# Kernel optimization log

Measured on AMD Instinct MI355X. Metric: run time of the kernel, lower is better.

## Reference

```python
import math
import jax, jax.numpy as jnp
import numpy as np

N_HEADS = 16
HIDDEN = 1024
FACTOR = 256
N_DK = HIDDEN // N_HEADS
B, S = 4, 2048


def _linear_params(key, fan_in, fan_out):
    kw, kb = jax.random.split(key)
    bound = 1.0 / math.sqrt(fan_in)
    W = jax.random.uniform(kw, (fan_in, fan_out), jnp.float32, -bound, bound)
    b = jax.random.uniform(kb, (fan_out,), jnp.float32, -bound, bound)
    return W, b


def setup_inputs() -> dict:
    key = jax.random.key(0)
    ks = jax.random.split(key, 12)
    inp = {
        "query": jax.random.normal(ks[0], (B, S, HIDDEN), jnp.float32),
        "key": jax.random.normal(ks[1], (B, S, HIDDEN), jnp.float32),
        "value": jax.random.normal(ks[2], (B, S, HIDDEN), jnp.float32),
        "mask": jax.random.randint(ks[3], (B, S), 0, 2, jnp.int32),
    }
    names = [("pq", HIDDEN, FACTOR), ("tq", FACTOR, HIDDEN),
             ("pk", HIDDEN, FACTOR), ("tk", FACTOR, HIDDEN),
             ("pv", HIDDEN, FACTOR), ("tv", FACTOR, HIDDEN),
             ("po", HIDDEN, FACTOR), ("to", FACTOR, HIDDEN)]
    for i, (nm, fi, fo) in enumerate(names):
        W, b = _linear_params(ks[4 + i], fi, fo)
        inp[f"W{nm}"], inp[f"b{nm}"] = W, b
    return inp


def _factored(x, Wp, bp, Wt, bt):
    # proj -> leaky_relu(0.2) -> tran
    h = jax.nn.leaky_relu(x @ Wp + bp, negative_slope=0.2)
    return h @ Wt + bt


def reference(query, key, value, mask,
              Wpq, bpq, Wtq, btq, Wpk, bpk, Wtk, btk,
              Wpv, bpv, Wtv, btv, Wpo, bpo, Wto, bto):
    bsize = query.shape[0]

    def split_heads(x):  # [B,S,H*Dk] -> [B,H,S,Dk]
        return x.reshape(bsize, -1, N_HEADS, N_DK).transpose(0, 2, 1, 3)

    q = split_heads(_factored(query, Wpq, bpq, Wtq, btq))
    k = split_heads(_factored(key, Wpk, bpk, Wtk, btk))
    v = split_heads(_factored(value, Wpv, bpv, Wtv, btv))

    scores = jnp.einsum("bhqd,bhkd->bhqk", q, k) / math.sqrt(N_DK)
    m = (mask == 0)[:, None, None, :]  # [B,1,1,S]
    scores = jnp.where(m, jnp.float32(-1e20), scores)
    attn = jax.nn.softmax(scores, axis=-1)
    cv = jnp.einsum("bhqk,bhkd->bhqd", attn, v)
    cv = cv.transpose(0, 2, 1, 3).reshape(bsize, -1, N_HEADS * N_DK)
    # dropout omitted (eval mode / deterministic reference)
    return _factored(cv, Wpo, bpo, Wto, bto)
```

## Files before the change

kernel.cpp:

```cpp
#include <hip/hip_runtime.h>
#include <cstdint>
#include <cstddef>

typedef __bf16 bf16_t;
typedef __bf16 bf16x8 __attribute__((ext_vector_type(8)));
typedef float  f32x4  __attribute__((ext_vector_type(4)));
typedef unsigned int uint32x4 __attribute__((ext_vector_type(4)));

#define DEV_INLINE __device__ __forceinline__

constexpr int Bsz = 4, Ssz = 2048, HID = 1024, FAC = 256, NH = 16, DKc = 64;
constexpr int Mrows = Bsz * Ssz;
constexpr float QSCALE = 0.18033688011112042f;

struct Ptr8 { const float* p[8]; };
struct Ptr3 { const float* p[3]; };

DEV_INLINE float fast_exp2(float x) {
#if __has_builtin(__builtin_amdgcn_exp2f)
  return __builtin_amdgcn_exp2f(x);
#else
  return exp2f(x);
#endif
}

DEV_INLINE void async16(const void* g, void* l) {
  __builtin_amdgcn_global_load_lds((const __attribute__((address_space(1))) void*)g,
                                   (__attribute__((address_space(3))) void*)l, 16, 0, 0);
}

DEV_INLINE int SW(int r) { return (r & 3) | ((r >> 1) & 4); }

__global__ __launch_bounds__(256) void k_prep_w(Ptr8 s, bf16_t* wpt, bf16_t* wtt) {
  const int z = blockIdx.z;
  const int K = (z < 4) ? HID : FAC;
  const int N = (z < 4) ? FAC : HID;
  if ((int)(blockIdx.x * 32) >= N || (int)(blockIdx.y * 32) >= K) return;
  __shared__ float t[32][33];
  const float* src = s.p[z];
  bf16_t* dst = (z < 4) ? (wpt + (size_t)z * FAC * HID) : (wtt + (size_t)(z - 4) * FAC * HID);
  const int tx = threadIdx.x & 31, ty = threadIdx.x >> 5;
  const int kb = blockIdx.y * 32, nb = blockIdx.x * 32;
#pragma unroll
  for (int j = 0; j < 4; ++j)
    t[ty + j * 8][tx] = src[(size_t)(kb + ty + j * 8) * N + nb + tx];
  __syncthreads();
#pragma unroll
  for (int j = 0; j < 4; ++j)
    dst[(size_t)(nb + ty + j * 8) * K + kb + tx] = (bf16_t)t[tx][ty + j * 8];
}

__global__ __launch_bounds__(256) void k_pack_bias(Ptr8 s, const int* __restrict__ mask,
                                                   float* bp, float* bt, float* mf, bf16_t* mb) {
  const int tid = threadIdx.x;
  for (int i = tid; i < 4 * FAC; i += 256) bp[i] = s.p[i >> 8][i & 255];
  for (int i = tid; i < 4 * HID; i += 256) bt[i] = s.p[4 + (i >> 10)][i & 1023];
  for (int i = tid; i < Bsz * Ssz; i += 256) {
    const float m = (mask[i] != 0) ? 1.f : 0.f;
    mf[i] = m;
    mb[i] = (bf16_t)m;
  }
}

__global__ __launch_bounds__(256) void k_tv(const bf16_t* __restrict__ src, bf16_t* __restrict__ dst) {
  constexpr int LDT = 72;
  __shared__ __align__(16) bf16_t T[64 * LDT];
  const int st = blockIdx.x, h = blockIdx.y, b = blockIdx.z;
  const int tid = threadIdx.x;
  const int sr = tid >> 3, sc8 = (tid & 7) * 8;
  const size_t g0 = (size_t)(b * Ssz + st * 64 + sr) * HID + h * DKc + sc8;
  *(uint32x4*)(T + sr * LDT + sc8) = *(const uint32x4*)(src + g0);
  *(uint32x4*)(T + (sr + 32) * LDT + sc8) = *(const uint32x4*)(src + g0 + (size_t)32 * HID);
  __syncthreads();
  union { bf16_t e[8]; uint32x4 u; } o0, o1;
#pragma unroll
  for (int j = 0; j < 8; ++j) {
    o0.e[j] = T[(sc8 + j) * LDT + sr];
    o1.e[j] = T[(sc8 + j) * LDT + sr + 32];
  }
  const size_t d0 = ((size_t)(b * NH + h) * DKc + sr) * Ssz + st * 64 + sc8;
  *(uint32x4*)(dst + d0) = o0.u;
  *(uint32x4*)(dst + d0 + (size_t)32 * Ssz) = o1.u;
}

template <int CAST_A, int ACT, int RM, typename OUT_T>
__global__ __launch_bounds__(256) void k_gemm(Ptr3 Asrc,
                                              const bf16_t* __restrict__ Aall,
                                              const bf16_t* __restrict__ Btall,
                                              const float* __restrict__ biasAll,
                                              OUT_T* __restrict__ Call,
                                              OUT_T* __restrict__ C2,
                                              const float* __restrict__ rowmul,
                                              int N, int K,
                                              long long Az, long long Bz, long long Cz, int biasz,
                                              float sc0, float sc1, float sc2) {
  constexpr int LDTA = CAST_A ? 40 : 32;
  __shared__ __align__(16) bf16_t As[128 * LDTA];
  __shared__ __align__(16) bf16_t Bs[128 * 32];

  const int z = blockIdx.z;
  const bf16_t* Bt = Btall + (size_t)z * Bz;
  const float* bias = biasAll + (size_t)z * biasz;
  OUT_T* C = (z == 2 && C2) ? C2 : (Call + (size_t)z * Cz);
  const float scale = (z == 0) ? sc0 : ((z == 1) ? sc1 : sc2);

  const int tid = threadIdx.x;
  const int lane = tid & 63, wave = tid >> 6;
  const int quad = lane >> 4, l16 = lane & 15;
  const int wr = wave >> 1, wc = wave & 1;
  const int m0 = blockIdx.y * 128, n0 = blockIdx.x * 128;

  const int arow = wave * 16 + (lane >> 2), akc = (lane & 3) * 8;
  const bf16_t* gB0 = Bt + (size_t)(n0 + arow) * K + akc;
  const bf16_t* gB1 = gB0 + (size_t)64 * K;
  bf16_t* lB0 = Bs + wave * 512;
  bf16_t* lB1 = Bs + 2048 + wave * 512;

  const bf16_t* gA0 = nullptr; const bf16_t* gA1 = nullptr;
  bf16_t* lA0 = As + wave * 512;
  bf16_t* lA1 = As + 2048 + wave * 512;
  const float* gAf = nullptr;
  bf16_t* lAc = nullptr;
  if (CAST_A) {
    const int crow = tid >> 1, chalf = (tid & 1) * 16;
    gAf = Asrc.p[z] + (size_t)(m0 + crow) * K + chalf;
    lAc = As + crow * LDTA + chalf;
  } else {
    const bf16_t* A = Aall + (size_t)z * Az;
    gA0 = A + (size_t)(m0 + arow) * K + akc;
    gA1 = gA0 + (size_t)64 * K;
  }

  f32x4 acc[4][4] = {};

  for (int k0 = 0; k0 < K; k0 += 32) {
    async16(gB0 + k0, lB0);
    async16(gB1 + k0, lB1);
    if (CAST_A) {
      f32x4 x0 = *(const f32x4*)(gAf + k0);
      f32x4 x1 = *(const f32x4*)(gAf + k0 + 4);
      f32x4 x2 = *(const f32x4*)(gAf + k0 + 8);
      f32x4 x3 = *(const f32x4*)(gAf + k0 + 12);
      union { bf16_t h[16]; uint32x4 u[2]; } o;
#pragma unroll
      for (int j = 0; j < 4; ++j) {
        o.h[j] = (bf16_t)x0[j]; o.h[4 + j] = (bf16_t)x1[j];
        o.h[8 + j] = (bf16_t)x2[j]; o.h[12 + j] = (bf16_t)x3[j];
      }
      *(uint32x4*)lAc = o.u[0];
      *(uint32x4*)(lAc + 8) = o.u[1];
    } else {
      async16(gA0 + k0, lA0);
      async16(gA1 + k0, lA1);
    }
    __syncthreads();

    bf16x8 af[4], bfr[4];
#pragma unroll
    for (int i = 0; i < 4; ++i)
      af[i] = *(const bf16x8*)(As + (wr * 64 + i * 16 + l16) * LDTA + quad * 8);
#pragma unroll
    for (int i = 0; i < 4; ++i)
      bfr[i] = *(const bf16x8*)(Bs + (wc * 64 + i * 16 + l16) * 32 + quad * 8);
#pragma unroll
    for (int mi = 0; mi < 4; ++mi)
#pragma unroll
      for (int ni = 0; ni < 4; ++ni)
        acc[mi][ni] = __builtin_amdgcn_mfma_f32_16x16x32_bf16(af[mi], bfr[ni], acc[mi][ni], 0, 0, 0);
    if (k0 + 32 < K) __syncthreads();
  }

#pragma unroll
  for (int mi = 0; mi < 4; ++mi) {
    const int rbase = m0 + wr * 64 + mi * 16 + quad * 4;
    float rmv[4] = {1.f, 1.f, 1.f, 1.f};
    if (RM && z == 2) {
#pragma unroll
      for (int r = 0; r < 4; ++r) rmv[r] = rowmul[rbase + r];
    }
#pragma unroll
    for (int ni = 0; ni < 4; ++ni) {
      const int col = n0 + wc * 64 + ni * 16 + l16;
      const float bv = bias[col];
#pragma unroll
      for (int r = 0; r < 4; ++r) {
        float y = acc[mi][ni][r] + bv;
        if (ACT == 1) y = (y > 0.f) ? y : 0.2f * y;
        y *= scale * rmv[r];
        C[(size_t)(rbase + r) * N + col] = (OUT_T)y;
      }
    }
  }
}

__global__ __launch_bounds__(256, 4) void k_attn(const bf16_t* __restrict__ qkv,
                                                 const bf16_t* __restrict__ mb,
                                                 bf16_t* __restrict__ cv) {
  __shared__ __align__(16) bf16_t Ks[2][64 * 64];
  __shared__ __align__(16) bf16_t Vt[2][64 * 64];
  __shared__ __align__(16) bf16_t Ml[Ssz];

  const int qt = blockIdx.x, h = blockIdx.y, b = blockIdx.z;
  const bf16_t* qp = qkv;
  const bf16_t* kp = qkv + (size_t)Mrows * HID;
  const bf16_t* vtp = qkv + 2 * (size_t)Mrows * HID + (size_t)(b * NH + h) * DKc * Ssz;

  const int tid = threadIdx.x;
  const int lane = tid & 63, wave = tid >> 6;
  const int quad = lane >> 4, l16 = lane & 15;

  const int r0 = wave * 16 + (lane >> 3);
  const int r1 = r0 + 8;
  const int c0 = ((lane & 7) ^ SW(r0)) * 8;
  const int c1 = ((lane & 7) ^ SW(r1)) * 8;
  const int ldsOff = wave * 1024;
  const bf16_t* kgA = kp + (size_t)(b * Ssz + r0) * HID + h * DKc + c0;
  const bf16_t* kgB = kp + (size_t)(b * Ssz + r1) * HID + h * DKc + c1;
  const bf16_t* vgA = vtp + (size_t)r0 * Ssz + c0;
  const bf16_t* vgB = vtp + (size_t)r1 * Ssz + c1;

  *(uint32x4*)(Ml + tid * 8) = *(const uint32x4*)(mb + (size_t)b * Ssz + tid * 8);
  async16(kgA, Ks[0] + ldsOff);
  async16(kgB, Ks[0] + ldsOff + 512);
  async16(vgA, Vt[0] + ldsOff);
  async16(vgB, Vt[0] + ldsOff + 512);

  bf16x8 aq0[2], aq1[2];
#pragma unroll
  for (int g = 0; g < 2; ++g) {
    const size_t qrow = (size_t)(b * Ssz + qt * 128 + g * 64 + wave * 16 + l16) * HID + h * DKc + quad * 8;
    aq0[g] = *(const bf16x8*)(qp + qrow);
    aq1[g] = *(const bf16x8*)(qp + qrow + 32);
  }
  __syncthreads();

  const int krow = 8 * (l16 >> 2) + (l16 & 3);
  f32x4 acc[2][4] = {};
  f32x4 dacc[2] = {};
  const bf16x8 zfrag = {};

  for (int kt = 0; kt < 32; ++kt) {
    const int cur = kt & 1, nxt = cur ^ 1;
    if (kt < 31) {
      const size_t ko = (size_t)(kt + 1) * 64 * HID;
      const int vo = (kt + 1) * 64;
      async16(kgA + ko, Ks[nxt] + ldsOff);
      async16(kgB + ko, Ks[nxt] + ldsOff + 512);
      async16(vgA + vo, Vt[nxt] + ldsOff);
      async16(vgB + vo, Vt[nxt] + ldsOff + 512);
    }

    uint32_t pk[2][8];
    constexpr int koff[4] = {0, 4, 32, 36};
#pragma unroll
    for (int ks = 0; ks < 4; ++ks) {
      const int row = krow + koff[ks];
      const int sw = SW(row);
      bf16x8 a0 = *(const bf16x8*)(Ks[cur] + row * 64 + (quad ^ sw) * 8);
      bf16x8 a1 = *(const bf16x8*)(Ks[cur] + row * 64 + ((quad + 4) ^ sw) * 8);
#pragma unroll
      for (int g = 0; g < 2; ++g) {
        f32x4 c = {};
        c = __builtin_amdgcn_mfma_f32_16x16x32_bf16(a0, aq0[g], c, 0, 0, 0);
        c = __builtin_amdgcn_mfma_f32_16x16x32_bf16(a1, aq1[g], c, 0, 0, 0);
        union { bf16_t h[2]; uint32_t u; } p01, p23;
        p01.h[0] = (bf16_t)fast_exp2(c[0]);
        p01.h[1] = (bf16_t)fast_exp2(c[1]);
        p23.h[0] = (bf16_t)fast_exp2(c[2]);
        p23.h[1] = (bf16_t)fast_exp2(c[3]);
        pk[g][ks * 2] = p01.u;
        pk[g][ks * 2 + 1] = p23.u;
      }
    }
    union { uint32x4 u; bf16x8 h; } ap0[2], ap1[2];
#pragma unroll
    for (int g = 0; g < 2; ++g) {
      ap0[g].u = uint32x4{pk[g][0], pk[g][1], pk[g][2], pk[g][3]};
      ap1[g].u = uint32x4{pk[g][4], pk[g][5], pk[g][6], pk[g][7]};
    }

    bf16x8 mr0 = *(const bf16x8*)(Ml + kt * 64 + quad * 8);
    bf16x8 mr1 = *(const bf16x8*)(Ml + kt * 64 + 32 + quad * 8);
    if (l16 != 0) { mr0 = zfrag; mr1 = zfrag; }
#pragma unroll
    for (int g = 0; g < 2; ++g) {
      dacc[g] = __builtin_amdgcn_mfma_f32_16x16x32_bf16(ap0[g].h, mr0, dacc[g], 0, 0, 0);
      dacc[g] = __builtin_amdgcn_mfma_f32_16x16x32_bf16(ap1[g].h, mr1, dacc[g], 0, 0, 0);
    }

#pragma unroll
    for (int d = 0; d < 4; ++d) {
      const int row = d * 16 + l16;
      const int sw = SW(row);
      bf16x8 bv0 = *(const bf16x8*)(Vt[cur] + row * 64 + (quad ^ sw) * 8);
      bf16x8 bv1 = *(const bf16x8*)(Vt[cur] + row * 64 + ((quad + 4) ^ sw) * 8);
#pragma unroll
      for (int g = 0; g < 2; ++g) {
        acc[g][d] = __builtin_amdgcn_mfma_f32_16x16x32_bf16(ap0[g].h, bv0, acc[g][d], 0, 0, 0);
        acc[g][d] = __builtin_amdgcn_mfma_f32_16x16x32_bf16(ap1[g].h, bv1, acc[g][d], 0, 0, 0);
      }
    }

    __syncthreads();
  }

#pragma unroll
  for (int g = 0; g < 2; ++g) {
    const size_t obase = (size_t)(b * Ssz + qt * 128 + g * 64 + wave * 16 + quad * 4) * HID + h * DKc + l16;
#pragma unroll
    for (int r = 0; r < 4; ++r) {
      const float denom = __shfl(dacc[g][r], lane & 48, 64);
      const float rl = 1.f / denom;
#pragma unroll
      for (int d = 0; d < 4; ++d)
        cv[obase + (size_t)r * HID + d * 16] = (bf16_t)(acc[g][d][r] * rl);
    }
  }
}

extern "C" void kernel_launch(void* const* d_in, const int* in_sizes, int n_in,
                              void* d_out, int out_size, void* d_ws, size_t ws_size,
                              hipStream_t stream) {
  (void)in_sizes; (void)n_in; (void)out_size; (void)ws_size;
  const float* q_in = (const float*)d_in[0];
  const float* k_in = (const float*)d_in[1];
  const float* v_in = (const float*)d_in[2];
  const int* mask = (const int*)d_in[3];

  bf16_t* XB = (bf16_t*)d_ws;
  bf16_t* H3 = XB + (size_t)3 * Mrows * HID;
  bf16_t* CV = H3 + (size_t)3 * Mrows * FAC;
  bf16_t* WPT = CV + (size_t)Mrows * HID;
  bf16_t* WTT = WPT + (size_t)4 * FAC * HID;
  float* BP = (float*)(WTT + (size_t)4 * FAC * HID);
  float* BT = BP + 4 * FAC;
  float* MF = BT + 4 * HID;
  bf16_t* MB = (bf16_t*)(MF + Mrows);
  bf16_t* VTg = XB + 2 * (size_t)Mrows * HID;

  Ptr8 w;
  w.p[0] = (const float*)d_in[4];  w.p[1] = (const float*)d_in[8];
  w.p[2] = (const float*)d_in[12]; w.p[3] = (const float*)d_in[16];
  w.p[4] = (const float*)d_in[6];  w.p[5] = (const float*)d_in[10];
  w.p[6] = (const float*)d_in[14]; w.p[7] = (const float*)d_in[18];
  hipLaunchKernelGGL(k_prep_w, dim3(32, 32, 8), dim3(256), 0, stream, w, WPT, WTT);

  Ptr8 bs;
  bs.p[0] = (const float*)d_in[5];  bs.p[1] = (const float*)d_in[9];
  bs.p[2] = (const float*)d_in[13]; bs.p[3] = (const float*)d_in[17];
  bs.p[4] = (const float*)d_in[7];  bs.p[5] = (const float*)d_in[11];
  bs.p[6] = (const float*)d_in[15]; bs.p[7] = (const float*)d_in[19];
  hipLaunchKernelGGL(k_pack_bias, dim3(1), dim3(256), 0, stream, bs, mask, BP, BT, MF, MB);

  Ptr3 xs; xs.p[0] = q_in; xs.p[1] = k_in; xs.p[2] = v_in;
  Ptr3 nullp; nullp.p[0] = nullp.p[1] = nullp.p[2] = nullptr;

  hipLaunchKernelGGL((k_gemm<1, 1, 0, bf16_t>), dim3(FAC / 128, Mrows / 128, 3), dim3(256), 0, stream,
                     xs, (const bf16_t*)nullptr, WPT, BP, H3, (bf16_t*)nullptr, (const float*)nullptr,
                     FAC, HID, 0LL, (long long)FAC * HID, (long long)Mrows * FAC, FAC,
                     1.f, 1.f, 1.f);

  hipLaunchKernelGGL((k_gemm<0, 0, 1, bf16_t>), dim3(HID / 128, Mrows / 128, 3), dim3(256), 0, stream,
                     nullp, H3, WTT, BT, XB, CV, MF,
                     HID, FAC, (long long)Mrows * FAC, (long long)FAC * HID, (long long)Mrows * HID, HID,
                     QSCALE, 1.f, 1.f);

  hipLaunchKernelGGL(k_tv, dim3(Ssz / 64, NH, Bsz), dim3(256), 0, stream, CV, VTg);

  hipLaunchKernelGGL(k_attn, dim3(Ssz / 128, NH, Bsz), dim3(256), 0, stream, XB, MB, CV);

  hipLaunchKernelGGL((k_gemm<0, 1, 0, bf16_t>), dim3(FAC / 128, Mrows / 128, 1), dim3(256), 0, stream,
                     nullp, CV, WPT + (size_t)3 * FAC * HID, BP + 3 * FAC, H3, (bf16_t*)nullptr,
                     (const float*)nullptr, FAC, HID, 0LL, 0LL, 0LL, 0, 1.f, 1.f, 1.f);

  hipLaunchKernelGGL((k_gemm<0, 0, 0, float>), dim3(HID / 128, Mrows / 128, 1), dim3(256), 0, stream,
                     nullp, H3, WTT + (size_t)3 * FAC * HID, BT + 3 * HID, (float*)d_out, (float*)nullptr,
                     (const float*)nullptr, HID, FAC, 0LL, 0LL, 0LL, 0, 1.f, 1.f, 1.f);
}
```

Before: 378.9 us.

## Add double-buffered 64-row GEMM for K=1024 projections and parallelize bias packing

```diff
diff --git a/kernel.cpp b/kernel.cpp
--- a/kernel.cpp
+++ b/kernel.cpp
@@ -52,10 +52,10 @@
 
 __global__ __launch_bounds__(256) void k_pack_bias(Ptr8 s, const int* __restrict__ mask,
                                                    float* bp, float* bt, float* mf, bf16_t* mb) {
-  const int tid = threadIdx.x;
-  for (int i = tid; i < 4 * FAC; i += 256) bp[i] = s.p[i >> 8][i & 255];
-  for (int i = tid; i < 4 * HID; i += 256) bt[i] = s.p[4 + (i >> 10)][i & 1023];
-  for (int i = tid; i < Bsz * Ssz; i += 256) {
+  const int i = blockIdx.x * 256 + threadIdx.x;
+  if (i < 4 * FAC) bp[i] = s.p[i >> 8][i & 255];
+  if (i < 4 * HID) bt[i] = s.p[4 + (i >> 10)][i & 1023];
+  if (i < Bsz * Ssz) {
     const float m = (mask[i] != 0) ? 1.f : 0.f;
     mf[i] = m;
     mb[i] = (bf16_t)m;
@@ -83,9 +83,111 @@
   *(uint32x4*)(dst + d0 + (size_t)32 * Ssz) = o1.u;
 }
 
-template <int CAST_A, int ACT, int RM, typename OUT_T>
-__global__ __launch_bounds__(256) void k_gemm(Ptr3 Asrc,
-                                              const bf16_t* __restrict__ Aall,
+template <int CAST_A, typename OUT_T>
+__global__ __launch_bounds__(256) void k_gemmP(Ptr3 Asrc,
+                                               const bf16_t* __restrict__ Aall,
+                                               const bf16_t* __restrict__ Bt_,
+                                               const float* __restrict__ biasAll,
+                                               OUT_T* __restrict__ Call,
+                                               int K,
+                                               long long Az, long long Bz, long long Cz, int biasz) {
+  constexpr int LDTA = CAST_A ? 40 : 32;
+  __shared__ __align__(16) bf16_t As[2][64 * LDTA];
+  __shared__ __align__(16) bf16_t Bs[2][128 * 32];
+
+  const int z = blockIdx.z;
+  const bf16_t* Bt = Bt_ + (size_t)z * Bz;
+  const float* bias = biasAll + (size_t)z * biasz;
+  OUT_T* C = Call + (size_t)z * Cz;
+
+  const int tid = threadIdx.x;
+  const int lane = tid & 63, wave = tid >> 6;
+  const int quad = lane >> 4, l16 = lane & 15;
+  const int m0 = blockIdx.y * 64, n0 = blockIdx.x * 128;
+
+  const int arow = wave * 16 + (lane >> 2), akc = (lane & 3) * 8;
+  const bf16_t* gB0 = Bt + (size_t)(n0 + arow) * K + akc;
+  const bf16_t* gB1 = gB0 + (size_t)64 * K;
+
+  const float* gAf = nullptr;
+  const bf16_t* gA = nullptr;
+  const int crow = tid >> 2, chalf = (tid & 3) * 8;
+  if (CAST_A) gAf = Asrc.p[z] + (size_t)(m0 + crow) * K + chalf;
+  else        gA  = Aall + (size_t)z * Az + (size_t)(m0 + arow) * K + akc;
+
+  async16(gB0, Bs[0] + wave * 512);
+  async16(gB1, Bs[0] + 2048 + wave * 512);
+  if (CAST_A) {
+    f32x4 x0 = *(const f32x4*)gAf;
+    f32x4 x1 = *(const f32x4*)(gAf + 4);
+    union { bf16_t h[8]; uint32x4 u; } o;
+#pragma unroll
+    for (int j = 0; j < 4; ++j) { o.h[j] = (bf16_t)x0[j]; o.h[4 + j] = (bf16_t)x1[j]; }
+    *(uint32x4*)(As[0] + crow * LDTA + chalf) = o.u;
+  } else {
+    async16(gA, As[0] + wave * 512);
+  }
+
+  f32x4 acc[4][2] = {};
+  const int nk = K / 32;
+
+  for (int it = 0; it < nk; ++it) {
+    const int cur = it & 1, nxt = cur ^ 1;
+    __syncthreads();
+
+    f32x4 xa, xb;
+    const int k1 = (it + 1) * 32;
+    if (it + 1 < nk) {
+      async16(gB0 + k1, Bs[nxt] + wave * 512);
+      async16(gB1 + k1, Bs[nxt] + 2048 + wave * 512);
+      if (CAST_A) {
+        xa = *(const f32x4*)(gAf + k1);
+        xb = *(const f32x4*)(gAf + k1 + 4);
+      } else {
+        async16(gA + k1, As[nxt] + wave * 512);
+      }
+    }
+
+    bf16x8 af[4], bfr[2];
+#pragma unroll
+    for (int i = 0; i < 4; ++i)
+      af[i] = *(const bf16x8*)(As[cur] + (i * 16 + l16) * LDTA + quad * 8);
+#pragma unroll
+    for (int i = 0; i < 2; ++i)
+      bfr[i] = *(const bf16x8*)(Bs[cur] + (wave * 32 + i * 16 + l16) * 32 + quad * 8);
+#pragma unroll
+    for (int mi = 0; mi < 4; ++mi)
+#pragma unroll
+      for (int ni = 0; ni < 2; ++ni)
+        acc[mi][ni] = __builtin_amdgcn_mfma_f32_16x16x32_bf16(af[mi], bfr[ni], acc[mi][ni], 0, 0, 0);
+
+    if (CAST_A && it + 1 < nk) {
+      union { bf16_t h[8]; uint32x4 u; } o;
+#pragma unroll
+      for (int j = 0; j < 4; ++j) { o.h[j] = (bf16_t)xa[j]; o.h[4 + j] = (bf16_t)xb[j]; }
+      *(uint32x4*)(As[nxt] + crow * LDTA + chalf) = o.u;
+    }
+  }
+
+#pragma unroll
+  for (int mi = 0; mi < 4; ++mi) {
+    const int rbase = m0 + mi * 16 + quad * 4;
+#pragma unroll
+    for (int ni = 0; ni < 2; ++ni) {
+      const int col = n0 + wave * 32 + ni * 16 + l16;
+      const float bv = bias[col];
+#pragma unroll
+      for (int r = 0; r < 4; ++r) {
+        float y = acc[mi][ni][r] + bv;
+        y = (y > 0.f) ? y : 0.2f * y;
+        C[(size_t)(rbase + r) * FAC + col] = (OUT_T)y;
+      }
+    }
+  }
+}
+
+template <int ACT, int RM, typename OUT_T>
+__global__ __launch_bounds__(256) void k_gemm(const bf16_t* __restrict__ Aall,
                                               const bf16_t* __restrict__ Btall,
                                               const float* __restrict__ biasAll,
                                               OUT_T* __restrict__ Call,
@@ -94,8 +196,7 @@
                                               int N, int K,
                                               long long Az, long long Bz, long long Cz, int biasz,
                                               float sc0, float sc1, float sc2) {
-  constexpr int LDTA = CAST_A ? 40 : 32;
-  __shared__ __align__(16) bf16_t As[128 * LDTA];
+  __shared__ __align__(16) bf16_t As[128 * 32];
   __shared__ __align__(16) bf16_t Bs[128 * 32];
 
   const int z = blockIdx.z;
@@ -116,49 +217,25 @@
   bf16_t* lB0 = Bs + wave * 512;
   bf16_t* lB1 = Bs + 2048 + wave * 512;
 
-  const bf16_t* gA0 = nullptr; const bf16_t* gA1 = nullptr;
+  const bf16_t* A = Aall + (size_t)z * Az;
+  const bf16_t* gA0 = A + (size_t)(m0 + arow) * K + akc;
+  const bf16_t* gA1 = gA0 + (size_t)64 * K;
   bf16_t* lA0 = As + wave * 512;
   bf16_t* lA1 = As + 2048 + wave * 512;
-  const float* gAf = nullptr;
-  bf16_t* lAc = nullptr;
-  if (CAST_A) {
-    const int crow = tid >> 1, chalf = (tid & 1) * 16;
-    gAf = Asrc.p[z] + (size_t)(m0 + crow) * K + chalf;
-    lAc = As + crow * LDTA + chalf;
-  } else {
-    const bf16_t* A = Aall + (size_t)z * Az;
-    gA0 = A + (size_t)(m0 + arow) * K + akc;
-    gA1 = gA0 + (size_t)64 * K;
-  }
 
   f32x4 acc[4][4] = {};
 
   for (int k0 = 0; k0 < K; k0 += 32) {
     async16(gB0 + k0, lB0);
     async16(gB1 + k0, lB1);
-    if (CAST_A) {
-      f32x4 x0 = *(const f32x4*)(gAf + k0);
-      f32x4 x1 = *(const f32x4*)(gAf + k0 + 4);
-      f32x4 x2 = *(const f32x4*)(gAf + k0 + 8);
-      f32x4 x3 = *(const f32x4*)(gAf + k0 + 12);
-      union { bf16_t h[16]; uint32x4 u[2]; } o;
-#pragma unroll
-      for (int j = 0; j < 4; ++j) {
-        o.h[j] = (bf16_t)x0[j]; o.h[4 + j] = (bf16_t)x1[j];
-        o.h[8 + j] = (bf16_t)x2[j]; o.h[12 + j] = (bf16_t)x3[j];
-      }
-      *(uint32x4*)lAc = o.u[0];
-      *(uint32x4*)(lAc + 8) = o.u[1];
-    } else {
-      async16(gA0 + k0, lA0);
-      async16(gA1 + k0, lA1);
-    }
+    async16(gA0 + k0, lA0);
+    async16(gA1 + k0, lA1);
     __syncthreads();
 
     bf16x8 af[4], bfr[4];
 #pragma unroll
     for (int i = 0; i < 4; ++i)
-      af[i] = *(const bf16x8*)(As + (wr * 64 + i * 16 + l16) * LDTA + quad * 8);
+      af[i] = *(const bf16x8*)(As + (wr * 64 + i * 16 + l16) * 32 + quad * 8);
 #pragma unroll
     for (int i = 0; i < 4; ++i)
       bfr[i] = *(const bf16x8*)(Bs + (wc * 64 + i * 16 + l16) * 32 + quad * 8);
@@ -350,18 +427,17 @@
   bs.p[2] = (const float*)d_in[13]; bs.p[3] = (const float*)d_in[17];
   bs.p[4] = (const float*)d_in[7];  bs.p[5] = (const float*)d_in[11];
   bs.p[6] = (const float*)d_in[15]; bs.p[7] = (const float*)d_in[19];
-  hipLaunchKernelGGL(k_pack_bias, dim3(1), dim3(256), 0, stream, bs, mask, BP, BT, MF, MB);
+  hipLaunchKernelGGL(k_pack_bias, dim3(64), dim3(256), 0, stream, bs, mask, BP, BT, MF, MB);
 
   Ptr3 xs; xs.p[0] = q_in; xs.p[1] = k_in; xs.p[2] = v_in;
   Ptr3 nullp; nullp.p[0] = nullp.p[1] = nullp.p[2] = nullptr;
 
-  hipLaunchKernelGGL((k_gemm<1, 1, 0, bf16_t>), dim3(FAC / 128, Mrows / 128, 3), dim3(256), 0, stream,
-                     xs, (const bf16_t*)nullptr, WPT, BP, H3, (bf16_t*)nullptr, (const float*)nullptr,
-                     FAC, HID, 0LL, (long long)FAC * HID, (long long)Mrows * FAC, FAC,
-                     1.f, 1.f, 1.f);
-
-  hipLaunchKernelGGL((k_gemm<0, 0, 1, bf16_t>), dim3(HID / 128, Mrows / 128, 3), dim3(256), 0, stream,
-                     nullp, H3, WTT, BT, XB, CV, MF,
+  hipLaunchKernelGGL((k_gemmP<1, bf16_t>), dim3(2, Mrows / 64, 3), dim3(256), 0, stream,
+                     xs, (const bf16_t*)nullptr, WPT, BP, H3,
+                     HID, 0LL, (long long)FAC * HID, (long long)Mrows * FAC, FAC);
+
+  hipLaunchKernelGGL((k_gemm<0, 1, bf16_t>), dim3(HID / 128, Mrows / 128, 3), dim3(256), 0, stream,
+                     H3, WTT, BT, XB, CV, MF,
                      HID, FAC, (long long)Mrows * FAC, (long long)FAC * HID, (long long)Mrows * HID, HID,
                      QSCALE, 1.f, 1.f);
 
@@ -369,11 +445,11 @@
 
   hipLaunchKernelGGL(k_attn, dim3(Ssz / 128, NH, Bsz), dim3(256), 0, stream, XB, MB, CV);
 
-  hipLaunchKernelGGL((k_gemm<0, 1, 0, bf16_t>), dim3(FAC / 128, Mrows / 128, 1), dim3(256), 0, stream,
-                     nullp, CV, WPT + (size_t)3 * FAC * HID, BP + 3 * FAC, H3, (bf16_t*)nullptr,
-                     (const float*)nullptr, FAC, HID, 0LL, 0LL, 0LL, 0, 1.f, 1.f, 1.f);
-
-  hipLaunchKernelGGL((k_gemm<0, 0, 0, float>), dim3(HID / 128, Mrows / 128, 1), dim3(256), 0, stream,
-                     nullp, H3, WTT + (size_t)3 * FAC * HID, BT + 3 * HID, (float*)d_out, (float*)nullptr,
+  hipLaunchKernelGGL((k_gemmP<0, bf16_t>), dim3(2, Mrows / 64, 1), dim3(256), 0, stream,
+                     nullp, CV, WPT + (size_t)3 * FAC * HID, BP + 3 * FAC, H3,
+                     HID, 0LL, 0LL, 0LL, 0);
+
+  hipLaunchKernelGGL((k_gemm<0, 0, float>), dim3(HID / 128, Mrows / 128, 1), dim3(256), 0, stream,
+                     H3, WTT + (size_t)3 * FAC * HID, BT + 3 * HID, (float*)d_out, (float*)nullptr,
                      (const float*)nullptr, HID, FAC, 0LL, 0LL, 0LL, 0, 1.f, 1.f, 1.f);
 }
```

Measured after the change: 353.6 us. 6.7% less time.
